# Performance work log

Measured on AMD Instinct MI355X. Metric: run time of the kernel, lower is better.

Reference implementation:

```python
import jax, jax.numpy as jnp
import numpy as np

B_SZ, SEQ, D_MODEL, D_STATE = 4, 4096, 1024, 16
LN_EPS = 1e-5


def setup_inputs() -> dict:
    key = jax.random.key(0)
    ks = jax.random.split(key, 6)
    x = jax.random.normal(ks[0], (B_SZ, SEQ, D_MODEL), jnp.float32)
    # A_log ~ U(-3, -1) per _init_weights
    A_log = jax.random.uniform(ks[1], (D_MODEL, D_STATE), jnp.float32, -3.0, -1.0)
    # xavier-ish init for projections
    B_w = jax.random.normal(ks[2], (D_STATE, D_MODEL), jnp.float32) / np.sqrt(D_MODEL)
    C_w = jax.random.normal(ks[3], (D_STATE, D_MODEL), jnp.float32) / np.sqrt(D_MODEL)
    D = jnp.ones((D_MODEL,), jnp.float32)
    gate_w = jax.random.normal(ks[4], (D_MODEL, D_MODEL), jnp.float32) / np.sqrt(D_MODEL)
    gate_b = jnp.zeros((D_MODEL,), jnp.float32)
    ln_gamma = jnp.ones((D_MODEL,), jnp.float32)
    ln_beta = jnp.zeros((D_MODEL,), jnp.float32)
    return {"x": x, "A_log": A_log, "B_w": B_w, "C_w": C_w, "D": D,
            "gate_w": gate_w, "gate_b": gate_b,
            "ln_gamma": ln_gamma, "ln_beta": ln_beta}


def reference(x, A_log, B_w, C_w, D, gate_w, gate_b, ln_gamma, ln_beta):
    b, s, d = x.shape
    n = A_log.shape[1]
    A = jnp.exp(A_log)                      # [d, n]
    Bx = jnp.einsum('bsd,nd->bsn', x, B_w)  # input-dependent B_t
    Cx = jnp.einsum('bsd,nd->bsn', x, C_w)  # input-dependent C_t

    def step(h, inp):
        x_t, B_t, C_t = inp                 # [b,d], [b,n], [b,n]
        h = h * A[None] + B_t[:, None, :] * x_t[:, :, None]   # [b,d,n]
        y_t = jnp.einsum('bdn,bn->bd', h, C_t) + D * x_t
        return h, y_t

    h0 = jnp.zeros((b, d, n), x.dtype)
    xs = (jnp.swapaxes(x, 0, 1), jnp.swapaxes(Bx, 0, 1), jnp.swapaxes(Cx, 0, 1))
    _, ys = jax.lax.scan(step, h0, xs)      # ys: [s,b,d]
    y = jnp.swapaxes(ys, 0, 1)              # [b,s,d]

    gate = jax.nn.sigmoid(jnp.einsum('bsd,ed->bse', x, gate_w) + gate_b)
    out = gate * y + (1.0 - gate) * x

    mu = jnp.mean(out, axis=-1, keepdims=True)
    var = jnp.var(out, axis=-1, keepdims=True)
    out = (out - mu) * jax.lax.rsqrt(var + LN_EPS) * ln_gamma + ln_beta
    # dropout is identity in eval mode
    return out
```

## Files before the change

### kernel.cpp

```cpp
#include <hip/hip_runtime.h>

#define B_SZ 4
#define SEQ  4096
#define DM   1024
#define DSTATE 16
#define ROWS (B_SZ*SEQ)

typedef unsigned short u16;
typedef __attribute__((ext_vector_type(8))) short   s16x8;
typedef __attribute__((ext_vector_type(4))) float   f32x4;
typedef __attribute__((ext_vector_type(4))) u16     u16x4;

__device__ inline float bf2f(u16 u) {
    unsigned v = ((unsigned)u) << 16;
    float f; __builtin_memcpy(&f, &v, 4); return f;
}
__device__ inline u16 f2bf(float f) {
    unsigned u; __builtin_memcpy(&u, &f, 4);
    return (u16)((u + 0x7FFFu + ((u >> 16) & 1u)) >> 16);
}
__device__ inline f32x4 mfma16(s16x8 a, s16x8 b, f32x4 c) {
    return __builtin_amdgcn_mfma_f32_16x16x32_bf16(a, b, c, 0, 0, 0);
}
__device__ inline void gl_lds16(const u16* g, u16* l) {
    __builtin_amdgcn_global_load_lds(
        (const __attribute__((address_space(1))) unsigned int*)g,
        (__attribute__((address_space(3))) unsigned int*)l, 16, 0, 0);
}

__global__ __launch_bounds__(256) void k_cvt_split(
    const float* __restrict__ in, u16* __restrict__ oh, u16* __restrict__ ol, int n4)
{
    int i = blockIdx.x * 256 + threadIdx.x;
    if (i < n4) {
        f32x4 v = ((const f32x4*)in)[i];
        u16x4 h, l;
#pragma unroll
        for (int c = 0; c < 4; c++) {
            h[c] = f2bf(v[c]);
            l[c] = f2bf(v[c] - bf2f(h[c]));
        }
        ((u16x4*)oh)[i] = h;
        ((u16x4*)ol)[i] = l;
    }
}

__global__ __launch_bounds__(256) void k_cvt_w(
    const float* __restrict__ gw, const float* __restrict__ Bw,
    const float* __restrict__ Cw, u16* __restrict__ gwb,
    u16* __restrict__ bwh, u16* __restrict__ bwl,
    u16* __restrict__ cwh, u16* __restrict__ cwl)
{
    int blk = blockIdx.x;
    if (blk < 1024) {
        int i = blk * 256 + threadIdx.x;
        f32x4 v = ((const f32x4*)gw)[i];
        u16x4 o;
#pragma unroll
        for (int c = 0; c < 4; c++) o[c] = f2bf(v[c]);
        ((u16x4*)gwb)[i] = o;
    } else {
        int isC = (blk >= 1040);
        const float* src = isC ? Cw : Bw;
        u16* dh = isC ? cwh : bwh;
        u16* dl = isC ? cwl : bwl;
        int i = (blk - (isC ? 1040 : 1024)) * 256 + threadIdx.x;
        f32x4 v = ((const f32x4*)src)[i];
        u16x4 h, l;
#pragma unroll
        for (int c = 0; c < 4; c++) {
            h[c] = f2bf(v[c]);
            l[c] = f2bf(v[c] - bf2f(h[c]));
        }
        ((u16x4*)dh)[i] = h;
        ((u16x4*)dl)[i] = l;
    }
}

__global__ __launch_bounds__(64) void k_bxcx(
    const u16* __restrict__ xh, const u16* __restrict__ xl,
    const u16* __restrict__ bwh, const u16* __restrict__ bwl,
    const u16* __restrict__ cwh, const u16* __restrict__ cwl,
    float* __restrict__ Bx, float* __restrict__ Cx)
{
    int lane = threadIdx.x;
    int lo = lane & 15, hi = lane >> 4;
    int m0 = blockIdx.x * 16;
    f32x4 accB = {}, accC = {};
    for (int k0 = 0; k0 < DM; k0 += 32) {
        size_t woff = (size_t)lo * DM + k0 + hi * 8;
        s16x8 bh = *(const s16x8*)(bwh + woff);
        s16x8 bl = *(const s16x8*)(bwl + woff);
        s16x8 ch = *(const s16x8*)(cwh + woff);
        s16x8 cl = *(const s16x8*)(cwl + woff);
        size_t aoff = (size_t)(m0 + lo) * DM + k0 + hi * 8;
        s16x8 ah = *(const s16x8*)(xh + aoff);
        s16x8 al = *(const s16x8*)(xl + aoff);
        accB = mfma16(ah, bh, accB);
        accB = mfma16(al, bh, accB);
        accB = mfma16(ah, bl, accB);
        accC = mfma16(ah, ch, accC);
        accC = mfma16(al, ch, accC);
        accC = mfma16(ah, cl, accC);
    }
#pragma unroll
    for (int r = 0; r < 4; r++) {
        int m = m0 + hi * 4 + r;
        Bx[(size_t)m * DSTATE + lo] = accB[r];
        Cx[(size_t)m * DSTATE + lo] = accC[r];
    }
}

#define BM 128
#define BN 128
#define BK 64

__global__ __launch_bounds__(256) void k_gate(
    const u16* __restrict__ xh, const u16* __restrict__ gwb,
    const float* __restrict__ gb, float* __restrict__ gate)
{
    __shared__ u16 sA[BM * BK], sB[BN * BK];
    int tid = threadIdx.x;
    int wv = tid >> 6, lane = tid & 63;
    int lo = lane & 15, hi = lane >> 4;
    int m0 = blockIdx.x * BM;
    int n0 = blockIdx.y * BN;

    int r_in = lane >> 3;
    int p    = lane & 7;
    int c    = p ^ r_in;

    int mrow = (wv & 1) * 64;
    int ncol = (wv >> 1) * 64;

    f32x4 acc[4][4] = {};
    for (int k0 = 0; k0 < DM; k0 += BK) {
        __syncthreads();
#pragma unroll
        for (int q = 0; q < 4; q++) {
            int r = (wv * 4 + q) * 8 + r_in;
            size_t goff = (size_t)r * DM + k0 + c * 8;
            gl_lds16(xh  + (size_t)m0 * DM + goff, &sA[(wv * 4 + q) * 512]);
            gl_lds16(gwb + (size_t)n0 * DM + goff, &sB[(wv * 4 + q) * 512]);
        }
        __syncthreads();
#pragma unroll
        for (int kk = 0; kk < 2; kk++) {
            s16x8 bfr[4], afr[4];
#pragma unroll
            for (int j = 0; j < 4; j++) {
                int rb = ncol + j * 16 + lo;
                int pc = (kk * 4 + hi) ^ (rb & 7);
                bfr[j] = *(const s16x8*)&sB[rb * BK + pc * 8];
            }
#pragma unroll
            for (int i = 0; i < 4; i++) {
                int ra = mrow + i * 16 + lo;
                int pc = (kk * 4 + hi) ^ (ra & 7);
                afr[i] = *(const s16x8*)&sA[ra * BK + pc * 8];
            }
#pragma unroll
            for (int i = 0; i < 4; i++)
#pragma unroll
                for (int j = 0; j < 4; j++)
                    acc[i][j] = mfma16(afr[i], bfr[j], acc[i][j]);
        }
    }
#pragma unroll
    for (int i = 0; i < 4; i++)
#pragma unroll
        for (int r = 0; r < 4; r++) {
            int m = m0 + mrow + i * 16 + hi * 4 + r;
#pragma unroll
            for (int j = 0; j < 4; j++) {
                int n = n0 + ncol + j * 16 + lo;
                float v = acc[i][j][r] + gb[n];
                gate[(size_t)m * DM + n] = 1.0f / (1.0f + __expf(-v));
            }
        }
}

#define CHUNK_L 64
#define LOOKBACK 32

__global__ __launch_bounds__(256) void k_scan(
    const float* __restrict__ x, const float* __restrict__ A_log,
    const float* __restrict__ Bx, const float* __restrict__ Cx,
    const float* __restrict__ Dvec, float* gate_out)
{
    __shared__ float sBx[(CHUNK_L + LOOKBACK) * DSTATE];
    __shared__ float sCx[(CHUNK_L + LOOKBACK) * DSTATE];
    int d = blockIdx.x * 256 + threadIdx.x;
    int b = blockIdx.z;
    int t0 = blockIdx.y * CHUNK_L;
    int tstart = t0 - LOOKBACK; if (tstart < 0) tstart = 0;
    int lb = t0 - tstart;
    int nv = (lb + CHUNK_L) * (DSTATE / 4);

    const f32x4* gB = (const f32x4*)(Bx + ((size_t)b * SEQ + tstart) * DSTATE);
    const f32x4* gC = (const f32x4*)(Cx + ((size_t)b * SEQ + tstart) * DSTATE);
    for (int i = threadIdx.x; i < nv; i += 256) {
        ((f32x4*)sBx)[i] = gB[i];
        ((f32x4*)sCx)[i] = gC[i];
    }

    float A[DSTATE], h[DSTATE];
    const f32x4* ga = (const f32x4*)(A_log + (size_t)d * DSTATE);
#pragma unroll
    for (int q = 0; q < 4; q++) {
        f32x4 av = ga[q];
#pragma unroll
        for (int c = 0; c < 4; c++) {
            A[q * 4 + c] = expf(av[c]);
            h[q * 4 + c] = 0.0f;
        }
    }
    float Dd = Dvec[d];
    __syncthreads();

    const float* xp = x + (size_t)(b * SEQ + tstart) * DM + d;

    for (int u = 0; u < lb; u += 4) {
        float xv[4];
#pragma unroll
        for (int q = 0; q < 4; q++) xv[q] = xp[(size_t)(u + q) * DM];
#pragma unroll
        for (int q = 0; q < 4; q++) {
            int idx = u + q;
#pragma unroll
            for (int n = 0; n < DSTATE; n++)
                h[n] = h[n] * A[n] + sBx[idx * DSTATE + n] * xv[q];
        }
    }

    float* gp = gate_out + (size_t)(b * SEQ + t0) * DM + d;
    const float* xp2 = x + (size_t)(b * SEQ + t0) * DM + d;
    for (int u = 0; u < CHUNK_L; u += 4) {
        float xv[4], gv[4], ov[4];
#pragma unroll
        for (int q = 0; q < 4; q++) {
            xv[q] = xp2[(size_t)(u + q) * DM];
            gv[q] = gp [(size_t)(u + q) * DM];
        }
#pragma unroll
        for (int q = 0; q < 4; q++) {
            int idx = lb + u + q;
            float y = 0.0f;
#pragma unroll
            for (int n = 0; n < DSTATE; n++) {
                h[n] = h[n] * A[n] + sBx[idx * DSTATE + n] * xv[q];
                y += h[n] * sCx[idx * DSTATE + n];
            }
            float yv = y + Dd * xv[q];
            ov[q] = gv[q] * yv + (1.0f - gv[q]) * xv[q];
        }
#pragma unroll
        for (int q = 0; q < 4; q++) gp[(size_t)(u + q) * DM] = ov[q];
    }
}

__global__ __launch_bounds__(256) void k_ln(
    float* data, const float* __restrict__ gamma, const float* __restrict__ beta)
{
    int wv = threadIdx.x >> 6, lane = threadIdx.x & 63;
    int row = blockIdx.x * 4 + wv;
    f32x4* rp = (f32x4*)(data + (size_t)row * DM);
    f32x4 v[4];
#pragma unroll
    for (int j = 0; j < 4; j++) v[j] = rp[lane + 64 * j];
    float s = 0.0f, s2 = 0.0f;
#pragma unroll
    for (int j = 0; j < 4; j++)
#pragma unroll
        for (int c = 0; c < 4; c++) { float t = v[j][c]; s += t; s2 += t * t; }
#pragma unroll
    for (int off = 32; off > 0; off >>= 1) {
        s  += __shfl_down(s,  off);
        s2 += __shfl_down(s2, off);
    }
    s = __shfl(s, 0); s2 = __shfl(s2, 0);
    float mu  = s  * (1.0f / DM);
    float var = s2 * (1.0f / DM) - mu * mu;
    float rs  = rsqrtf(var + 1e-5f);
#pragma unroll
    for (int j = 0; j < 4; j++) {
        int c0 = (lane + 64 * j) * 4;
        f32x4 o;
#pragma unroll
        for (int c = 0; c < 4; c++)
            o[c] = (v[j][c] - mu) * rs * gamma[c0 + c] + beta[c0 + c];
        rp[lane + 64 * j] = o;
    }
}

extern "C" void kernel_launch(void* const* d_in, const int* in_sizes, int n_in,
                              void* d_out, int out_size, void* d_ws, size_t ws_size,
                              hipStream_t stream)
{
    const float* x     = (const float*)d_in[0];
    const float* A_log = (const float*)d_in[1];
    const float* Bw    = (const float*)d_in[2];
    const float* Cw    = (const float*)d_in[3];
    const float* Dv    = (const float*)d_in[4];
    const float* gw    = (const float*)d_in[5];
    const float* gb    = (const float*)d_in[6];
    const float* gam   = (const float*)d_in[7];
    const float* bet   = (const float*)d_in[8];
    float* out = (float*)d_out;

    char* ws = (char*)d_ws;
    u16*   xh  = (u16*)  ws;
    u16*   xl  = (u16*)  (ws + (32u << 20));
    u16*   gwb = (u16*)  (ws + (64u << 20));
    u16*   bwh = (u16*)  (ws + (66u << 20));
    u16*   bwl = (u16*)  (ws + (66u << 20) + (32u << 10));
    u16*   cwh = (u16*)  (ws + (66u << 20) + (64u << 10));
    u16*   cwl = (u16*)  (ws + (66u << 20) + (96u << 10));
    float* Bx  = (float*)(ws + (67u << 20));
    float* Cx  = (float*)(ws + (68u << 20));

    k_cvt_split<<<ROWS * DM / 4 / 256, 256, 0, stream>>>(x, xh, xl, ROWS * DM / 4);
    k_cvt_w<<<1056, 256, 0, stream>>>(gw, Bw, Cw, gwb, bwh, bwl, cwh, cwl);
    k_bxcx<<<ROWS / 16, 64, 0, stream>>>(xh, xl, bwh, bwl, cwh, cwl, Bx, Cx);
    k_gate<<<dim3(ROWS / BM, DM / BN), 256, 0, stream>>>(xh, gwb, gb, out);
    k_scan<<<dim3(DM / 256, SEQ / CHUNK_L, B_SZ), 256, 0, stream>>>(
        x, A_log, Bx, Cx, Dv, out);
    k_ln<<<ROWS / 4, 256, 0, stream>>>(out, gam, bet);
}
```

Measured before the change: 278.5 us.

## Fuse scan with LayerNorm and store gate as bf16 in workspace

The scan kernel now covers all 1024 channels of a 64-step chunk per 1024-thread block. It stages 16 rows of gated output in LDS and applies LayerNorm in-block, writing final output directly. This removes the separate LN kernel and its full read-modify-write of the output tensor. The gate is stored as bf16 in the reused xl buffer, halving gate traffic at some precision cost. The fewer, larger blocks with 64KB+ shared memory and extra barriers may reduce occupancy.

```diff
diff --git a/kernel.cpp b/kernel.cpp
--- a/kernel.cpp
+++ b/kernel.cpp
@@ -117,7 +117,7 @@
 
 __global__ __launch_bounds__(256) void k_gate(
     const u16* __restrict__ xh, const u16* __restrict__ gwb,
-    const float* __restrict__ gb, float* __restrict__ gate)
+    const float* __restrict__ gb, u16* __restrict__ gate)
 {
     __shared__ u16 sA[BM * BK], sB[BN * BK];
     int tid = threadIdx.x;
@@ -175,33 +175,37 @@
             for (int j = 0; j < 4; j++) {
                 int n = n0 + ncol + j * 16 + lo;
                 float v = acc[i][j][r] + gb[n];
-                gate[(size_t)m * DM + n] = 1.0f / (1.0f + __expf(-v));
+                gate[(size_t)m * DM + n] = f2bf(1.0f / (1.0f + __expf(-v)));
             }
         }
 }
 
 #define CHUNK_L 64
 #define LOOKBACK 32
-
-__global__ __launch_bounds__(256) void k_scan(
+#define GROUP 16
+
+__global__ __launch_bounds__(1024, 4) void k_scan_ln(
     const float* __restrict__ x, const float* __restrict__ A_log,
     const float* __restrict__ Bx, const float* __restrict__ Cx,
-    const float* __restrict__ Dvec, float* gate_out)
+    const float* __restrict__ Dvec, const u16* __restrict__ gate,
+    const float* __restrict__ gamma, const float* __restrict__ beta,
+    float* __restrict__ out)
 {
     __shared__ float sBx[(CHUNK_L + LOOKBACK) * DSTATE];
     __shared__ float sCx[(CHUNK_L + LOOKBACK) * DSTATE];
-    int d = blockIdx.x * 256 + threadIdx.x;
-    int b = blockIdx.z;
-    int t0 = blockIdx.y * CHUNK_L;
+    __shared__ float sOut[GROUP * DM];
+    int d = threadIdx.x;
+    int b = blockIdx.y;
+    int t0 = blockIdx.x * CHUNK_L;
     int tstart = t0 - LOOKBACK; if (tstart < 0) tstart = 0;
     int lb = t0 - tstart;
     int nv = (lb + CHUNK_L) * (DSTATE / 4);
 
     const f32x4* gB = (const f32x4*)(Bx + ((size_t)b * SEQ + tstart) * DSTATE);
     const f32x4* gC = (const f32x4*)(Cx + ((size_t)b * SEQ + tstart) * DSTATE);
-    for (int i = threadIdx.x; i < nv; i += 256) {
-        ((f32x4*)sBx)[i] = gB[i];
-        ((f32x4*)sCx)[i] = gC[i];
+    if (threadIdx.x < nv) {
+        ((f32x4*)sBx)[threadIdx.x] = gB[threadIdx.x];
+        ((f32x4*)sCx)[threadIdx.x] = gC[threadIdx.x];
     }
 
     float A[DSTATE], h[DSTATE];
@@ -218,8 +222,7 @@
     float Dd = Dvec[d];
     __syncthreads();
 
-    const float* xp = x + (size_t)(b * SEQ + tstart) * DM + d;
-
+    const float* xp = x + ((size_t)b * SEQ + tstart) * DM + d;
     for (int u = 0; u < lb; u += 4) {
         float xv[4];
 #pragma unroll
@@ -233,63 +236,61 @@
         }
     }
 
-    float* gp = gate_out + (size_t)(b * SEQ + t0) * DM + d;
-    const float* xp2 = x + (size_t)(b * SEQ + t0) * DM + d;
-    for (int u = 0; u < CHUNK_L; u += 4) {
-        float xv[4], gv[4], ov[4];
-#pragma unroll
-        for (int q = 0; q < 4; q++) {
-            xv[q] = xp2[(size_t)(u + q) * DM];
-            gv[q] = gp [(size_t)(u + q) * DM];
-        }
-#pragma unroll
-        for (int q = 0; q < 4; q++) {
-            int idx = lb + u + q;
+    int w    = threadIdx.x >> 6;
+    int lane = threadIdx.x & 63;
+    for (int g = 0; g < CHUNK_L / GROUP; ++g) {
+        int tg0 = t0 + g * GROUP;
+        const float* xpg = x    + ((size_t)b * SEQ + tg0) * DM + d;
+        const u16*   gpg = gate + ((size_t)b * SEQ + tg0) * DM + d;
+        float xv[GROUP], gv[GROUP];
+#pragma unroll
+        for (int u = 0; u < GROUP; u++) xv[u] = xpg[(size_t)u * DM];
+#pragma unroll
+        for (int u = 0; u < GROUP; u++) gv[u] = bf2f(gpg[(size_t)u * DM]);
+#pragma unroll
+        for (int u = 0; u < GROUP; u++) {
+            int idx = lb + g * GROUP + u;
             float y = 0.0f;
 #pragma unroll
             for (int n = 0; n < DSTATE; n++) {
-                h[n] = h[n] * A[n] + sBx[idx * DSTATE + n] * xv[q];
+                h[n] = h[n] * A[n] + sBx[idx * DSTATE + n] * xv[u];
                 y += h[n] * sCx[idx * DSTATE + n];
             }
-            float yv = y + Dd * xv[q];
-            ov[q] = gv[q] * yv + (1.0f - gv[q]) * xv[q];
-        }
-#pragma unroll
-        for (int q = 0; q < 4; q++) gp[(size_t)(u + q) * DM] = ov[q];
-    }
-}
-
-__global__ __launch_bounds__(256) void k_ln(
-    float* data, const float* __restrict__ gamma, const float* __restrict__ beta)
-{
-    int wv = threadIdx.x >> 6, lane = threadIdx.x & 63;
-    int row = blockIdx.x * 4 + wv;
-    f32x4* rp = (f32x4*)(data + (size_t)row * DM);
-    f32x4 v[4];
-#pragma unroll
-    for (int j = 0; j < 4; j++) v[j] = rp[lane + 64 * j];
-    float s = 0.0f, s2 = 0.0f;
-#pragma unroll
-    for (int j = 0; j < 4; j++)
-#pragma unroll
-        for (int c = 0; c < 4; c++) { float t = v[j][c]; s += t; s2 += t * t; }
-#pragma unroll
-    for (int off = 32; off > 0; off >>= 1) {
-        s  += __shfl_down(s,  off);
-        s2 += __shfl_down(s2, off);
-    }
-    s = __shfl(s, 0); s2 = __shfl(s2, 0);
-    float mu  = s  * (1.0f / DM);
-    float var = s2 * (1.0f / DM) - mu * mu;
-    float rs  = rsqrtf(var + 1e-5f);
-#pragma unroll
-    for (int j = 0; j < 4; j++) {
-        int c0 = (lane + 64 * j) * 4;
-        f32x4 o;
-#pragma unroll
-        for (int c = 0; c < 4; c++)
-            o[c] = (v[j][c] - mu) * rs * gamma[c0 + c] + beta[c0 + c];
-        rp[lane + 64 * j] = o;
+            float yv = y + Dd * xv[u];
+            sOut[u * DM + d] = gv[u] * yv + (1.0f - gv[u]) * xv[u];
+        }
+        __syncthreads();
+        {
+            const float* sr = sOut + w * DM;
+            f32x4 v[4];
+#pragma unroll
+            for (int j = 0; j < 4; j++) v[j] = ((const f32x4*)sr)[lane + 64 * j];
+            float s = 0.0f, s2 = 0.0f;
+#pragma unroll
+            for (int j = 0; j < 4; j++)
+#pragma unroll
+                for (int c = 0; c < 4; c++) { float t = v[j][c]; s += t; s2 += t * t; }
+#pragma unroll
+            for (int off = 32; off > 0; off >>= 1) {
+                s  += __shfl_down(s,  off);
+                s2 += __shfl_down(s2, off);
+            }
+            s = __shfl(s, 0); s2 = __shfl(s2, 0);
+            float mu  = s  * (1.0f / DM);
+            float var = s2 * (1.0f / DM) - mu * mu;
+            float rs  = rsqrtf(var + 1e-5f);
+            float* op = out + ((size_t)b * SEQ + tg0 + w) * DM;
+#pragma unroll
+            for (int j = 0; j < 4; j++) {
+                int c0 = (lane + 64 * j) * 4;
+                f32x4 o;
+#pragma unroll
+                for (int c = 0; c < 4; c++)
+                    o[c] = (v[j][c] - mu) * rs * gamma[c0 + c] + beta[c0 + c];
+                *(f32x4*)(op + c0) = o;
+            }
+        }
+        __syncthreads();
     }
 }
 
@@ -309,21 +310,21 @@
     float* out = (float*)d_out;
 
     char* ws = (char*)d_ws;
-    u16*   xh  = (u16*)  ws;
-    u16*   xl  = (u16*)  (ws + (32u << 20));
-    u16*   gwb = (u16*)  (ws + (64u << 20));
-    u16*   bwh = (u16*)  (ws + (66u << 20));
-    u16*   bwl = (u16*)  (ws + (66u << 20) + (32u << 10));
-    u16*   cwh = (u16*)  (ws + (66u << 20) + (64u << 10));
-    u16*   cwl = (u16*)  (ws + (66u << 20) + (96u << 10));
-    float* Bx  = (float*)(ws + (67u << 20));
-    float* Cx  = (float*)(ws + (68u << 20));
+    u16*   xh   = (u16*)  ws;
+    u16*   xl   = (u16*)  (ws + (32u << 20));
+    u16*   gate = xl;
+    u16*   gwb  = (u16*)  (ws + (64u << 20));
+    u16*   bwh  = (u16*)  (ws + (66u << 20));
+    u16*   bwl  = (u16*)  (ws + (66u << 20) + (32u << 10));
+    u16*   cwh  = (u16*)  (ws + (66u << 20) + (64u << 10));
+    u16*   cwl  = (u16*)  (ws + (66u << 20) + (96u << 10));
+    float* Bx   = (float*)(ws + (67u << 20));
+    float* Cx   = (float*)(ws + (68u << 20));
 
     k_cvt_split<<<ROWS * DM / 4 / 256, 256, 0, stream>>>(x, xh, xl, ROWS * DM / 4);
     k_cvt_w<<<1056, 256, 0, stream>>>(gw, Bw, Cw, gwb, bwh, bwl, cwh, cwl);
     k_bxcx<<<ROWS / 16, 64, 0, stream>>>(xh, xl, bwh, bwl, cwh, cwl, Bx, Cx);
-    k_gate<<<dim3(ROWS / BM, DM / BN), 256, 0, stream>>>(xh, gwb, gb, out);
-    k_scan<<<dim3(DM / 256, SEQ / CHUNK_L, B_SZ), 256, 0, stream>>>(
-        x, A_log, Bx, Cx, Dv, out);
-    k_ln<<<ROWS / 4, 256, 0, stream>>>(out, gam, bet);
-}
+    k_gate<<<dim3(ROWS / BM, DM / BN), 256, 0, stream>>>(xh, gwb, gb, gate);
+    k_scan_ln<<<dim3(SEQ / CHUNK_L, B_SZ), 1024, 0, stream>>>(
+        x, A_log, Bx, Cx, Dv, gate, gam, bet, out);
+}
```

Result: slower. 298.6 us (+7.2%).

## Split x in-register for Bx/Cx and store gate as bf16

Applied to the files above, without the earlier changes.

k_bxcx now reads fp32 x and splits it into bf16 hi/lo in registers, so the conversion kernel no longer writes a full-size low-part buffer. k_gate writes the sigmoid gate as bf16 into workspace instead of fp32 into the output, and k_scan reads that bf16 gate and writes its result to the output. Together these reduce HBM traffic (one 32MB write, one 32MB read, and half of the gate round trip). The cost is extra conversion arithmetic in k_bxcx, fp32 re-reads of x there, and reduced precision in the gate values.

```diff
diff --git a/kernel.cpp b/kernel.cpp
--- a/kernel.cpp
+++ b/kernel.cpp
@@ -28,20 +28,16 @@
         (__attribute__((address_space(3))) unsigned int*)l, 16, 0, 0);
 }
 
-__global__ __launch_bounds__(256) void k_cvt_split(
-    const float* __restrict__ in, u16* __restrict__ oh, u16* __restrict__ ol, int n4)
+__global__ __launch_bounds__(256) void k_cvt_xh(
+    const float* __restrict__ in, u16* __restrict__ oh, int n4)
 {
     int i = blockIdx.x * 256 + threadIdx.x;
     if (i < n4) {
         f32x4 v = ((const f32x4*)in)[i];
-        u16x4 h, l;
-#pragma unroll
-        for (int c = 0; c < 4; c++) {
-            h[c] = f2bf(v[c]);
-            l[c] = f2bf(v[c] - bf2f(h[c]));
-        }
+        u16x4 h;
+#pragma unroll
+        for (int c = 0; c < 4; c++) h[c] = f2bf(v[c]);
         ((u16x4*)oh)[i] = h;
-        ((u16x4*)ol)[i] = l;
     }
 }
 
@@ -78,7 +74,7 @@
 }
 
 __global__ __launch_bounds__(64) void k_bxcx(
-    const u16* __restrict__ xh, const u16* __restrict__ xl,
+    const float* __restrict__ x,
     const u16* __restrict__ bwh, const u16* __restrict__ bwl,
     const u16* __restrict__ cwh, const u16* __restrict__ cwl,
     float* __restrict__ Bx, float* __restrict__ Cx)
@@ -94,8 +90,15 @@
         s16x8 ch = *(const s16x8*)(cwh + woff);
         s16x8 cl = *(const s16x8*)(cwl + woff);
         size_t aoff = (size_t)(m0 + lo) * DM + k0 + hi * 8;
-        s16x8 ah = *(const s16x8*)(xh + aoff);
-        s16x8 al = *(const s16x8*)(xl + aoff);
+        f32x4 a0 = *(const f32x4*)(x + aoff);
+        f32x4 a1 = *(const f32x4*)(x + aoff + 4);
+        s16x8 ah, al;
+#pragma unroll
+        for (int c = 0; c < 4; c++) {
+            u16 t;
+            t = f2bf(a0[c]); ah[c] = (short)t;     al[c]     = (short)f2bf(a0[c] - bf2f(t));
+            t = f2bf(a1[c]); ah[c + 4] = (short)t; al[c + 4] = (short)f2bf(a1[c] - bf2f(t));
+        }
         accB = mfma16(ah, bh, accB);
         accB = mfma16(al, bh, accB);
         accB = mfma16(ah, bl, accB);
@@ -117,7 +120,7 @@
 
 __global__ __launch_bounds__(256) void k_gate(
     const u16* __restrict__ xh, const u16* __restrict__ gwb,
-    const float* __restrict__ gb, float* __restrict__ gate)
+    const float* __restrict__ gb, u16* __restrict__ gate)
 {
     __shared__ u16 sA[BM * BK], sB[BN * BK];
     int tid = threadIdx.x;
@@ -175,7 +178,7 @@
             for (int j = 0; j < 4; j++) {
                 int n = n0 + ncol + j * 16 + lo;
                 float v = acc[i][j][r] + gb[n];
-                gate[(size_t)m * DM + n] = 1.0f / (1.0f + __expf(-v));
+                gate[(size_t)m * DM + n] = f2bf(1.0f / (1.0f + __expf(-v)));
             }
         }
 }
@@ -186,7 +189,8 @@
 __global__ __launch_bounds__(256) void k_scan(
     const float* __restrict__ x, const float* __restrict__ A_log,
     const float* __restrict__ Bx, const float* __restrict__ Cx,
-    const float* __restrict__ Dvec, float* gate_out)
+    const float* __restrict__ Dvec, const u16* __restrict__ gate,
+    float* __restrict__ out_pre)
 {
     __shared__ float sBx[(CHUNK_L + LOOKBACK) * DSTATE];
     __shared__ float sCx[(CHUNK_L + LOOKBACK) * DSTATE];
@@ -218,7 +222,7 @@
     float Dd = Dvec[d];
     __syncthreads();
 
-    const float* xp = x + (size_t)(b * SEQ + tstart) * DM + d;
+    const float* xp = x + ((size_t)b * SEQ + tstart) * DM + d;
 
     for (int u = 0; u < lb; u += 4) {
         float xv[4];
@@ -233,14 +237,15 @@
         }
     }
 
-    float* gp = gate_out + (size_t)(b * SEQ + t0) * DM + d;
-    const float* xp2 = x + (size_t)(b * SEQ + t0) * DM + d;
+    const float* xp2 = x    + ((size_t)b * SEQ + t0) * DM + d;
+    const u16*   gp  = gate + ((size_t)b * SEQ + t0) * DM + d;
+    float*       op  = out_pre + ((size_t)b * SEQ + t0) * DM + d;
     for (int u = 0; u < CHUNK_L; u += 4) {
         float xv[4], gv[4], ov[4];
 #pragma unroll
         for (int q = 0; q < 4; q++) {
             xv[q] = xp2[(size_t)(u + q) * DM];
-            gv[q] = gp [(size_t)(u + q) * DM];
+            gv[q] = bf2f(gp[(size_t)(u + q) * DM]);
         }
 #pragma unroll
         for (int q = 0; q < 4; q++) {
@@ -255,7 +260,7 @@
             ov[q] = gv[q] * yv + (1.0f - gv[q]) * xv[q];
         }
 #pragma unroll
-        for (int q = 0; q < 4; q++) gp[(size_t)(u + q) * DM] = ov[q];
+        for (int q = 0; q < 4; q++) op[(size_t)(u + q) * DM] = ov[q];
     }
 }
 
@@ -309,21 +314,21 @@
     float* out = (float*)d_out;
 
     char* ws = (char*)d_ws;
-    u16*   xh  = (u16*)  ws;
-    u16*   xl  = (u16*)  (ws + (32u << 20));
-    u16*   gwb = (u16*)  (ws + (64u << 20));
-    u16*   bwh = (u16*)  (ws + (66u << 20));
-    u16*   bwl = (u16*)  (ws + (66u << 20) + (32u << 10));
-    u16*   cwh = (u16*)  (ws + (66u << 20) + (64u << 10));
-    u16*   cwl = (u16*)  (ws + (66u << 20) + (96u << 10));
-    float* Bx  = (float*)(ws + (67u << 20));
-    float* Cx  = (float*)(ws + (68u << 20));
-
-    k_cvt_split<<<ROWS * DM / 4 / 256, 256, 0, stream>>>(x, xh, xl, ROWS * DM / 4);
+    u16*   xh   = (u16*)  ws;
+    u16*   gate = (u16*)  (ws + (32u << 20));
+    u16*   gwb  = (u16*)  (ws + (64u << 20));
+    u16*   bwh  = (u16*)  (ws + (66u << 20));
+    u16*   bwl  = (u16*)  (ws + (66u << 20) + (32u << 10));
+    u16*   cwh  = (u16*)  (ws + (66u << 20) + (64u << 10));
+    u16*   cwl  = (u16*)  (ws + (66u << 20) + (96u << 10));
+    float* Bx   = (float*)(ws + (67u << 20));
+    float* Cx   = (float*)(ws + (68u << 20));
+
+    k_cvt_xh<<<ROWS * DM / 4 / 256, 256, 0, stream>>>(x, xh, ROWS * DM / 4);
     k_cvt_w<<<1056, 256, 0, stream>>>(gw, Bw, Cw, gwb, bwh, bwl, cwh, cwl);
-    k_bxcx<<<ROWS / 16, 64, 0, stream>>>(xh, xl, bwh, bwl, cwh, cwl, Bx, Cx);
-    k_gate<<<dim3(ROWS / BM, DM / BN), 256, 0, stream>>>(xh, gwb, gb, out);
+    k_bxcx<<<ROWS / 16, 64, 0, stream>>>(x, bwh, bwl, cwh, cwl, Bx, Cx);
+    k_gate<<<dim3(ROWS / BM, DM / BN), 256, 0, stream>>>(xh, gwb, gb, gate);
     k_scan<<<dim3(DM / 256, SEQ / CHUNK_L, B_SZ), 256, 0, stream>>>(
-        x, A_log, Bx, Cx, Dv, out);
+        x, A_log, Bx, Cx, Dv, gate, out);
     k_ln<<<ROWS / 4, 256, 0, stream>>>(out, gam, bet);
 }
```

Result: no change. 284.0 us (+2.0%).
